# Kernel tuning notes

Measured on AMD Instinct MI355X. Metric: run time of the kernel, lower is better.

Reference implementation:

```python
import jax, jax.numpy as jnp
import numpy as np

VOCAB = 32000
HIDDEN = 256
BATCH = 32
SEQ = 128


def setup_inputs() -> dict:
    key = jax.random.key(0)
    ks = jax.random.split(key, 9)
    stdv = 1.0 / np.sqrt(HIDDEN)
    tokens = jax.random.randint(ks[0], (BATCH, SEQ), 0, VOCAB)
    lengths = jax.random.randint(ks[1], (BATCH,), 1, SEQ + 1)
    emb = jax.random.normal(ks[2], (VOCAB, HIDDEN), dtype=jnp.float32)
    W_x1 = jax.random.uniform(ks[3], (HIDDEN, HIDDEN), jnp.float32, -stdv, stdv)
    W_h1 = jax.random.uniform(ks[4], (HIDDEN, HIDDEN), jnp.float32, -stdv, stdv)
    b1 = jnp.zeros((HIDDEN,), jnp.float32)
    W_x2 = jax.random.uniform(ks[5], (HIDDEN, HIDDEN), jnp.float32, -stdv, stdv)
    W_h2 = jax.random.uniform(ks[6], (HIDDEN, HIDDEN), jnp.float32, -stdv, stdv)
    b2 = jnp.zeros((HIDDEN,), jnp.float32)
    return {"tokens": tokens, "lengths": lengths, "emb": emb,
            "W_x1": W_x1, "W_h1": W_h1, "b1": b1,
            "W_x2": W_x2, "W_h2": W_h2, "b2": b2}


def _rnn_layer(x, W_x, W_h, b, mask):
    # x: [B,T,H] (already zeroed at padded positions, matching pad_packed_sequence)
    B = x.shape[0]
    h0 = jnp.zeros((B, W_h.shape[0]), x.dtype)

    def step(h, x_t):
        # torch: tanh(W_x @ x_t[...,None] + W_h @ h[...,None]).squeeze() + b)
        h = jnp.tanh(x_t @ W_x.T + h @ W_h.T + b)
        return h, h

    _, hs = jax.lax.scan(step, h0, jnp.swapaxes(x, 0, 1))  # [T,B,H]
    hs = jnp.swapaxes(hs, 0, 1)  # [B,T,H]
    # pack_padded_sequence drops padded steps -> zero them out
    return hs * mask[:, :, None]


def reference(tokens, lengths, emb, W_x1, W_h1, b1, W_x2, W_h2, b2):
    B, T = tokens.shape
    mask = (jnp.arange(T)[None, :] < lengths[:, None]).astype(emb.dtype)  # [B,T]
    # Model.forward: argmax of one-hot -> token ids -> embedding lookup
    x = emb[tokens] * mask[:, :, None]  # [B,T,H], padded positions are zeros
    h1 = _rnn_layer(x, W_x1, W_h1, b1, mask)
    h2 = _rnn_layer(h1, W_x2, W_h2, b2, mask)
    logits = h2 @ emb.T  # [B,T,V] tied output projection
    probs = jax.nn.softmax(logits, axis=-1) * mask[:, :, None]
    return probs, h2
```

## Files before the change

kernel.cpp:

```cpp
#include <hip/hip_runtime.h>
#include <hip/hip_bf16.h>

#define VOCAB 32000
#define HID   256
#define BATCH 32
#define SEQ   128
#define MROWS (BATCH * SEQ)
#define NCB   250

typedef _Float16 f16;
typedef _Float16 f16x4 __attribute__((ext_vector_type(4)));
typedef _Float16 f16x8 __attribute__((ext_vector_type(8)));
typedef float    f32x4 __attribute__((ext_vector_type(4)));

#define GLOAD_LDS16(gptr, lptr)                                                       \
  __builtin_amdgcn_global_load_lds(                                                   \
      (const __attribute__((address_space(1))) unsigned int*)(gptr),                  \
      (__attribute__((address_space(3))) unsigned int*)(lptr), 16, 0, 0)

__global__ __launch_bounds__(256) void embed_kernel(
    const int* __restrict__ tokens, const int* __restrict__ lengths,
    const float* __restrict__ emb, float* __restrict__ x) {
  int row = blockIdx.x;
  int b = row >> 7, t = row & 127;
  int tok = tokens[row];
  float v = (t < lengths[b]) ? emb[(size_t)tok * HID + threadIdx.x] : 0.f;
  x[(size_t)row * HID + threadIdx.x] = v;
}

__global__ __launch_bounds__(256) void cast_kernel(
    const float* __restrict__ in, f16* __restrict__ out, int n4) {
  int idx = blockIdx.x * 256 + threadIdx.x;
  if (idx >= n4) return;
  float4 v = ((const float4*)in)[idx];
  f16x4 o = {(f16)v.x, (f16)v.y, (f16)v.z, (f16)v.w};
  ((f16x4*)out)[idx] = o;
}

__global__ __launch_bounds__(256) void xprep_kernel(
    const float* __restrict__ In, const float* __restrict__ W,
    const float* __restrict__ bias, float* __restrict__ Out) {
  __shared__ float sIn[16 * 256];
  int tid = threadIdx.x;
  int rb = blockIdx.x * 16;
  const float4* g = (const float4*)(In + (size_t)rb * 256);
  float4* s4 = (float4*)sIn;
#pragma unroll
  for (int q = 0; q < 4; ++q) s4[tid + q * 256] = g[tid + q * 256];
  __syncthreads();
  int i = tid;
  float acc[16];
#pragma unroll
  for (int r = 0; r < 16; ++r) acc[r] = 0.f;
  const float4* w4 = (const float4*)(W + (size_t)i * 256);
#pragma unroll 4
  for (int j = 0; j < 64; ++j) {
    float4 wv = w4[j];
#pragma unroll
    for (int r = 0; r < 16; ++r) {
      float4 sv = ((const float4*)(sIn + r * 256))[j];
      acc[r] += sv.x * wv.x + sv.y * wv.y + sv.z * wv.z + sv.w * wv.w;
    }
  }
  float bi = bias[i];
#pragma unroll
  for (int r = 0; r < 16; ++r) Out[(size_t)(rb + r) * 256 + i] = acc[r] + bi;
}

__global__ __launch_bounds__(512) void rnn_kernel(
    const float* __restrict__ X, const float* __restrict__ Wh,
    const int* __restrict__ lengths, float* __restrict__ Hout) {
  int b = blockIdx.x;
  int tid = threadIdx.x;
  int i = tid & 255;
  int half = tid >> 8;
  float w[128];
  {
    const float4* wr = (const float4*)(Wh + (size_t)i * 256 + half * 128);
#pragma unroll
    for (int q = 0; q < 32; ++q) {
      float4 v = wr[q];
      w[4 * q + 0] = v.x; w[4 * q + 1] = v.y;
      w[4 * q + 2] = v.z; w[4 * q + 3] = v.w;
    }
  }
  __shared__ float sh[256];
  __shared__ float sp[256];
  if (tid < 256) sh[tid] = 0.f;
  int len = lengths[b];
  const float* Xb = X + (size_t)b * SEQ * HID;
  float* Hb = Hout + (size_t)b * SEQ * HID;
  __syncthreads();
  float xnext = (half == 0) ? Xb[i] : 0.f;
  for (int t = 0; t < SEQ; ++t) {
    float a0 = 0.f, a1 = 0.f, a2 = 0.f, a3 = 0.f;
    const float4* hp = (const float4*)(sh + half * 128);
#pragma unroll
    for (int q = 0; q < 32; ++q) {
      float4 hv = hp[q];
      a0 += hv.x * w[4 * q + 0];
      a1 += hv.y * w[4 * q + 1];
      a2 += hv.z * w[4 * q + 2];
      a3 += hv.w * w[4 * q + 3];
    }
    float acc = (a0 + a1) + (a2 + a3);
    if (half) sp[i] = acc;
    __syncthreads();
    if (!half) {
      float h = tanhf(xnext + acc + sp[i]);
      Hb[(size_t)t * HID + i] = (t < len) ? h : 0.f;
      sh[i] = h;
      if (t + 1 < SEQ) xnext = Xb[(size_t)(t + 1) * HID + i];
    }
    __syncthreads();
  }
}

template <int WRITE_PROBS>
__global__ __launch_bounds__(256) void gemm_kernel(
    const f16* __restrict__ A,
    const f16* __restrict__ Bm,
    float* __restrict__ C,
    float* __restrict__ PM,
    float* __restrict__ PL,
    const float* __restrict__ Mrow,
    const float* __restrict__ Inv,
    const int* __restrict__ lengths) {
  __shared__ __align__(16) f16 sA[128 * 64];
  __shared__ __align__(16) f16 sB[128 * 64];
  __shared__ float sM[128];
  __shared__ float sI[128];
  const int tid = threadIdx.x;
  const int wave = tid >> 6;
  const int lane = tid & 63;
  const int row0 = blockIdx.x * 128;
  const int col0 = blockIdx.y * 128;

  const int len = lengths[blockIdx.x];
  const int lenc = (len + 15) & ~15;

  if (WRITE_PROBS) {
    if (tid < 128) {
      sM[tid] = Mrow[row0 + tid];
      sI[tid] = Inv[row0 + tid];
    }
  }

  f32x4 acc[4][4];
#pragma unroll
  for (int a = 0; a < 4; ++a)
#pragma unroll
    for (int b = 0; b < 4; ++b) acc[a][b] = (f32x4){0.f, 0.f, 0.f, 0.f};

  const int lr = lane >> 3;
  const int ls = lane & 7;
  const int wm = wave & 1, wn = wave >> 1;

  for (int ko = 0; ko < 4; ++ko) {
#pragma unroll
    for (int ii = 0; ii < 4; ++ii) {
      int ar = wave * 32 + ii * 8;
      int r = ar + lr;
      int c = ls ^ (r & 7);
      if (ar < lenc) {
        const f16* ga = A + (size_t)(row0 + r) * 256 + ko * 64 + c * 8;
        GLOAD_LDS16(ga, sA + ar * 64);
      }
      const f16* gb = Bm + (size_t)(col0 + r) * 256 + ko * 64 + c * 8;
      GLOAD_LDS16(gb, sB + ar * 64);
    }
    __syncthreads();
#pragma unroll
    for (int kk = 0; kk < 2; ++kk) {
      const int cA = kk * 4 + (lane >> 4);
      f16x8 bf[4];
#pragma unroll
      for (int f = 0; f < 4; ++f) {
        int n = wn * 64 + f * 16 + (lane & 15);
        bf[f] = *(const f16x8*)(sB + n * 64 + (cA ^ (n & 7)) * 8);
      }
#pragma unroll
      for (int fm = 0; fm < 4; ++fm) {
        const int g = fm * 2 + wm;
        if (g * 16 < len) {
          int m = g * 16 + (lane & 15);
          f16x8 af = *(const f16x8*)(sA + m * 64 + (cA ^ (m & 7)) * 8);
#pragma unroll
          for (int fn = 0; fn < 4; ++fn)
            acc[fm][fn] = __builtin_amdgcn_mfma_f32_16x16x32_f16(
                af, bf[fn], acc[fm][fn], 0, 0, 0);
        }
      }
    }
    __syncthreads();
  }

  const int lq = lane >> 4;
  const int lc = lane & 15;

  if (WRITE_PROBS) {
#pragma unroll
    for (int fm = 0; fm < 4; ++fm)
#pragma unroll
      for (int fn = 0; fn < 4; ++fn)
#pragma unroll
        for (int rr = 0; rr < 4; ++rr) {
          int t = (fm * 2 + wm) * 16 + lq * 4 + rr;
          int col = col0 + wn * 64 + fn * 16 + lc;
          float v =
              (t < len) ? __expf(acc[fm][fn][rr] - sM[t]) * sI[t] : 0.f;
          C[(size_t)(row0 + t) * VOCAB + col] = v;
        }
  } else {
    float* rm = (float*)sA;
    float* rs = rm + 256;
#pragma unroll
    for (int fm = 0; fm < 4; ++fm) {
      const int g = fm * 2 + wm;
      const bool active = (g * 16 < len);
#pragma unroll
      for (int rr = 0; rr < 4; ++rr) {
        int r = g * 16 + lq * 4 + rr;
        if (active) {
          float mx = fmaxf(fmaxf(acc[fm][0][rr], acc[fm][1][rr]),
                           fmaxf(acc[fm][2][rr], acc[fm][3][rr]));
#pragma unroll
          for (int off = 1; off < 16; off <<= 1)
            mx = fmaxf(mx, __shfl_xor(mx, off, 64));
          float sum = __expf(acc[fm][0][rr] - mx) +
                      __expf(acc[fm][1][rr] - mx) +
                      __expf(acc[fm][2][rr] - mx) +
                      __expf(acc[fm][3][rr] - mx);
#pragma unroll
          for (int off = 1; off < 16; off <<= 1)
            sum += __shfl_xor(sum, off, 64);
          if (lc == 0) {
            rm[wn * 128 + r] = mx;
            rs[wn * 128 + r] = sum;
          }
        } else if (lc == 0) {
          rm[wn * 128 + r] = 0.f;
          rs[wn * 128 + r] = 0.f;
        }
      }
    }
    __syncthreads();
    if (tid < 128) {
      float m0 = rm[tid], m1 = rm[128 + tid];
      float M = fmaxf(m0, m1);
      float L = rs[tid] * __expf(m0 - M) + rs[128 + tid] * __expf(m1 - M);
      PM[(size_t)(row0 + tid) * NCB + blockIdx.y] = M;
      PL[(size_t)(row0 + tid) * NCB + blockIdx.y] = L;
    }
  }
}

__global__ __launch_bounds__(256) void combine_kernel(
    const float* __restrict__ PM, const float* __restrict__ PL,
    float* __restrict__ Mrow, float* __restrict__ Inv) {
  int row = blockIdx.x * 4 + (threadIdx.x >> 6);
  int lane = threadIdx.x & 63;
  const float* pm = PM + (size_t)row * NCB;
  const float* pl = PL + (size_t)row * NCB;
  float M = -3.4e38f;
  for (int i = lane; i < NCB; i += 64) M = fmaxf(M, pm[i]);
#pragma unroll
  for (int off = 1; off < 64; off <<= 1) M = fmaxf(M, __shfl_xor(M, off, 64));
  float L = 0.f;
  for (int i = lane; i < NCB; i += 64) L += pl[i] * __expf(pm[i] - M);
#pragma unroll
  for (int off = 1; off < 64; off <<= 1) L += __shfl_xor(L, off, 64);
  if (lane == 0) {
    Mrow[row] = M;
    Inv[row] = 1.f / L;
  }
}

extern "C" void kernel_launch(void* const* d_in, const int* in_sizes, int n_in,
                              void* d_out, int out_size, void* d_ws,
                              size_t ws_size, hipStream_t stream) {
  const int* tokens = (const int*)d_in[0];
  const int* lengths = (const int*)d_in[1];
  const float* emb = (const float*)d_in[2];
  const float* Wx1 = (const float*)d_in[3];
  const float* Wh1 = (const float*)d_in[4];
  const float* b1 = (const float*)d_in[5];
  const float* Wx2 = (const float*)d_in[6];
  const float* Wh2 = (const float*)d_in[7];
  const float* b2 = (const float*)d_in[8];

  float* probs = (float*)d_out;
  float* h2out = probs + (size_t)MROWS * VOCAB;

  float* ws = (float*)d_ws;
  float* x = ws;
  float* X = ws + 1048576;
  float* h1 = ws + 2097152;
  f16* embh = (f16*)(ws + 3145728);
  f16* h2h = (f16*)(ws + 3145728 + 4096000);
  float* PM = ws + 7766016;
  float* PL = ws + 8790016;
  float* Mrow = ws + 9814016;
  float* Inv = ws + 9818112;

  embed_kernel<<<MROWS, 256, 0, stream>>>(tokens, lengths, emb, x);
  cast_kernel<<<8000, 256, 0, stream>>>(emb, embh, VOCAB * HID / 4);

  xprep_kernel<<<256, 256, 0, stream>>>(x, Wx1, b1, X);
  rnn_kernel<<<BATCH, 512, 0, stream>>>(X, Wh1, lengths, h1);
  xprep_kernel<<<256, 256, 0, stream>>>(h1, Wx2, b2, X);
  rnn_kernel<<<BATCH, 512, 0, stream>>>(X, Wh2, lengths, h2out);

  cast_kernel<<<1024, 256, 0, stream>>>(h2out, h2h, MROWS * HID / 4);

  dim3 gg(32, NCB);
  gemm_kernel<0><<<gg, 256, 0, stream>>>(h2h, embh, nullptr, PM, PL,
                                         nullptr, nullptr, lengths);
  combine_kernel<<<MROWS / 4, 256, 0, stream>>>(PM, PL, Mrow, Inv);
  gemm_kernel<1><<<gg, 256, 0, stream>>>(h2h, embh, probs, nullptr, nullptr,
                                         Mrow, Inv, lengths);
}
```

Before: 1.064 ms.

## Double-buffer LDS tiles in logits GEMM and remap blocks across XCDs

The GEMM kernel now keeps two LDS buffers and issues the global-to-LDS loads for the next K-slice before computing on the current one, so memory latency can overlap with MFMA work. It also remaps the flat block index so that consecutive work items are spread across the 8 XCDs, with each XCD handling a contiguous range, which may improve L2 reuse of the embedding tiles. The softmax stats are now staged into the reused LDS after the main loop. LDS usage doubles, which can lower occupancy.

New measurement: 1.070 ms. No clear change (+0.5%).

```diff
diff --git a/kernel.cpp b/kernel.cpp
--- a/kernel.cpp
+++ b/kernel.cpp
@@ -126,25 +126,21 @@
     const float* __restrict__ Mrow,
     const float* __restrict__ Inv,
     const int* __restrict__ lengths) {
-  __shared__ __align__(16) f16 sA[128 * 64];
-  __shared__ __align__(16) f16 sB[128 * 64];
-  __shared__ float sM[128];
-  __shared__ float sI[128];
+  __shared__ __align__(16) f16 sAbuf[2][128 * 64];
+  __shared__ __align__(16) f16 sBbuf[2][128 * 64];
   const int tid = threadIdx.x;
   const int wave = tid >> 6;
   const int lane = tid & 63;
-  const int row0 = blockIdx.x * 128;
-  const int col0 = blockIdx.y * 128;
-
-  const int len = lengths[blockIdx.x];
+
+  const int flat = blockIdx.x + 32 * blockIdx.y;
+  const int work = (flat & 7) * 1000 + (flat >> 3);
+  const int bx = work & 31;
+  const int by = work >> 5;
+  const int row0 = bx * 128;
+  const int col0 = by * 128;
+
+  const int len = lengths[bx];
   const int lenc = (len + 15) & ~15;
-
-  if (WRITE_PROBS) {
-    if (tid < 128) {
-      sM[tid] = Mrow[row0 + tid];
-      sI[tid] = Inv[row0 + tid];
-    }
-  }
 
   f32x4 acc[4][4];
 #pragma unroll
@@ -156,20 +152,28 @@
   const int ls = lane & 7;
   const int wm = wave & 1, wn = wave >> 1;
 
+#define STAGE(buf, koo)                                                        \
+  {                                                                            \
+    _Pragma("unroll") for (int ii = 0; ii < 4; ++ii) {                         \
+      int ar = wave * 32 + ii * 8;                                             \
+      int r = ar + lr;                                                         \
+      int c = ls ^ (r & 7);                                                    \
+      if (ar < lenc) {                                                         \
+        const f16* ga = A + (size_t)(row0 + r) * 256 + (koo) * 64 + c * 8;     \
+        GLOAD_LDS16(ga, sAbuf[buf] + ar * 64);                                 \
+      }                                                                        \
+      const f16* gb = Bm + (size_t)(col0 + r) * 256 + (koo) * 64 + c * 8;      \
+      GLOAD_LDS16(gb, sBbuf[buf] + ar * 64);                                   \
+    }                                                                          \
+  }
+
+  STAGE(0, 0);
+  __syncthreads();
+
+#pragma unroll
   for (int ko = 0; ko < 4; ++ko) {
-#pragma unroll
-    for (int ii = 0; ii < 4; ++ii) {
-      int ar = wave * 32 + ii * 8;
-      int r = ar + lr;
-      int c = ls ^ (r & 7);
-      if (ar < lenc) {
-        const f16* ga = A + (size_t)(row0 + r) * 256 + ko * 64 + c * 8;
-        GLOAD_LDS16(ga, sA + ar * 64);
-      }
-      const f16* gb = Bm + (size_t)(col0 + r) * 256 + ko * 64 + c * 8;
-      GLOAD_LDS16(gb, sB + ar * 64);
-    }
-    __syncthreads();
+    const int cur = ko & 1;
+    if (ko < 3) STAGE(cur ^ 1, ko + 1);
 #pragma unroll
     for (int kk = 0; kk < 2; ++kk) {
       const int cA = kk * 4 + (lane >> 4);
@@ -177,14 +181,14 @@
 #pragma unroll
       for (int f = 0; f < 4; ++f) {
         int n = wn * 64 + f * 16 + (lane & 15);
-        bf[f] = *(const f16x8*)(sB + n * 64 + (cA ^ (n & 7)) * 8);
+        bf[f] = *(const f16x8*)(sBbuf[cur] + n * 64 + (cA ^ (n & 7)) * 8);
       }
 #pragma unroll
       for (int fm = 0; fm < 4; ++fm) {
         const int g = fm * 2 + wm;
         if (g * 16 < len) {
           int m = g * 16 + (lane & 15);
-          f16x8 af = *(const f16x8*)(sA + m * 64 + (cA ^ (m & 7)) * 8);
+          f16x8 af = *(const f16x8*)(sAbuf[cur] + m * 64 + (cA ^ (m & 7)) * 8);
 #pragma unroll
           for (int fn = 0; fn < 4; ++fn)
             acc[fm][fn] = __builtin_amdgcn_mfma_f32_16x16x32_f16(
@@ -194,11 +198,19 @@
     }
     __syncthreads();
   }
+#undef STAGE
 
   const int lq = lane >> 4;
   const int lc = lane & 15;
 
   if (WRITE_PROBS) {
+    float* sM = (float*)sAbuf;
+    float* sI = sM + 128;
+    if (tid < 128) {
+      sM[tid] = Mrow[row0 + tid];
+      sI[tid] = Inv[row0 + tid];
+    }
+    __syncthreads();
 #pragma unroll
     for (int fm = 0; fm < 4; ++fm)
 #pragma unroll
@@ -212,7 +224,7 @@
           C[(size_t)(row0 + t) * VOCAB + col] = v;
         }
   } else {
-    float* rm = (float*)sA;
+    float* rm = (float*)sAbuf;
     float* rs = rm + 256;
 #pragma unroll
     for (int fm = 0; fm < 4; ++fm) {
@@ -249,8 +261,8 @@
       float m0 = rm[tid], m1 = rm[128 + tid];
       float M = fmaxf(m0, m1);
       float L = rs[tid] * __expf(m0 - M) + rs[128 + tid] * __expf(m1 - M);
-      PM[(size_t)(row0 + tid) * NCB + blockIdx.y] = M;
-      PL[(size_t)(row0 + tid) * NCB + blockIdx.y] = L;
+      PM[(size_t)(row0 + tid) * NCB + by] = M;
+      PL[(size_t)(row0 + tid) * NCB + by] = L;
     }
   }
 }
```
